# Performance work log

Measured on AMD Instinct MI355X. Metric: run time of the kernel, lower is better.

## Reference

```python
import jax, jax.numpy as jnp
import numpy as np

N = 50000       # nodes
E = 800000      # directed edges (src -> dst)
INDIM, HID, OUT = 256, 128, 64
NEG_SLOPE = 0.2  # PyG GATConv default negative_slope


def gat_layer(x, src, dst, W, a_src, a_dst, b, n_nodes):
    """Single-head PyG-style GATConv with self-loops already in (src, dst)."""
    h = x @ W.T                                   # [N, F_out]
    alpha_src = h @ a_src                         # [N]
    alpha_dst = h @ a_dst                         # [N]
    # per-edge attention logits, LeakyReLU
    e = jax.nn.leaky_relu(alpha_src[src] + alpha_dst[dst], NEG_SLOPE)  # [E']
    # segment softmax grouped by destination node (numerically stable)
    m = jnp.full((n_nodes,), -jnp.inf, e.dtype).at[dst].max(e)
    ee = jnp.exp(e - m[dst])
    denom = jax.ops.segment_sum(ee, dst, num_segments=n_nodes)
    alpha = ee / denom[dst]                       # [E']
    # weighted scatter-add of source messages
    out = jax.ops.segment_sum(h[src] * alpha[:, None], dst, num_segments=n_nodes)
    return out + b


def setup_inputs() -> dict:
    key = jax.random.key(0)
    ks = jax.random.split(key, 10)
    s = 0.1
    return {
        "x": jax.random.normal(ks[0], (N, INDIM), jnp.float32),
        "edge_index": jax.random.randint(ks[1], (2, E), 0, N, dtype=jnp.int32),
        "W1": jax.random.normal(ks[2], (HID, INDIM), jnp.float32) * s,
        "a_src1": jax.random.normal(ks[3], (HID,), jnp.float32) * s,
        "a_dst1": jax.random.normal(ks[4], (HID,), jnp.float32) * s,
        "b1": jnp.zeros((HID,), jnp.float32),
        "W2": jax.random.normal(ks[5], (OUT, HID), jnp.float32) * s,
        "a_src2": jax.random.normal(ks[6], (OUT,), jnp.float32) * s,
        "a_dst2": jax.random.normal(ks[7], (OUT,), jnp.float32) * s,
        "b2": jnp.zeros((OUT,), jnp.float32),
    }


def reference(x, edge_index, W1, a_src1, a_dst1, b1, W2, a_src2, a_dst2, b2):
    n_nodes = x.shape[0]
    # PyG GATConv default add_self_loops=True
    loops = jnp.arange(n_nodes, dtype=edge_index.dtype)
    src = jnp.concatenate([edge_index[0], loops])
    dst = jnp.concatenate([edge_index[1], loops])
    h = gat_layer(x, src, dst, W1, a_src1, a_dst1, b1, n_nodes)
    h = jax.nn.relu(h)
    h = gat_layer(h, src, dst, W2, a_src2, a_dst2, b2, n_nodes)
    return h
```

## Files before the change

### kernel.cpp

```cpp
#include <hip/hip_runtime.h>
#include <hip/hip_bf16.h>
#include <math.h>

#define NN 50000
#define EE 800000
#define INDIM 256
#define HID 128
#define OUTF 64
#define NEG_SLOPE 0.2f
#define CAP 64

#define NB ((NN + 255) >> 8)
#define BCAP 6144
#define CHUNK 2048
#define EPT 8
#define BPAD 16

typedef __attribute__((ext_vector_type(8))) short bf16x8;
typedef __attribute__((ext_vector_type(4))) float f32x4;

__device__ inline float bflo(unsigned p) { return __uint_as_float(p << 16); }
__device__ inline float bfhi(unsigned p) { return __uint_as_float(p & 0xffff0000u); }
__device__ inline unsigned f2bf(float f) {
    unsigned u = __float_as_uint(f);
    return (u + 0x7fffu + ((u >> 16) & 1u)) >> 16;
}
__device__ inline unsigned cvt_pk_bf16(float lo, float hi) {
    unsigned r;
    asm("v_cvt_pk_bf16_f32 %0, %1, %2" : "=v"(r) : "v"(lo), "v"(hi));
    return r;
}
__device__ inline float leaky(float l) { return (l > 0.f) ? l : NEG_SLOPE * l; }

template <typename AT, int BM, int BN, int WR, int WC, bool FAL>
__device__ inline void gemm_body(const AT* __restrict__ A,
                                 const float* __restrict__ B,
                                 unsigned short* __restrict__ Cb,
                                 const float* __restrict__ a_s,
                                 const float* __restrict__ a_d,
                                 float* __restrict__ asrc,
                                 float* __restrict__ adst,
                                 int N, int K, int bid)
{
    constexpr int LD = 40;
    constexpr int MF = (BM / WR) / 16;
    constexpr int NF = (BN / WC) / 16;
    constexpr int NA  = (sizeof(AT) == 4) ? (BM * 8 / 256) : (BM * 4 / 256);
    constexpr int NBL = BN * 8 / 256;
    __shared__ unsigned short As[BM * LD];
    __shared__ unsigned short Bs[BN * LD];
    __shared__ float al_s[FAL ? 2 * BM : 2];

    const int tid = threadIdx.x;
    const int wave = tid >> 6, lane = tid & 63;
    const int wr = wave / WC, wc = wave % WC;
    const int wrow0 = wr * (BM / WR);
    const int wcol0 = wc * (BN / WC);
    const int row0 = bid * BM;
    const int lrow = lane & 15, lkg = lane >> 4;

    if constexpr (FAL) {
        for (int i = tid; i < 2 * BM; i += 256) al_s[i] = 0.f;
    }

    int arow[NA], aoff[NA]; bool aval[NA];
    #pragma unroll
    for (int u = 0; u < NA; ++u) {
        int i = u * 256 + tid;
        if constexpr (sizeof(AT) == 4) { arow[u] = i >> 3; aoff[u] = (i & 7) * 4; }
        else                           { arow[u] = i >> 2; aoff[u] = (i & 3) * 8; }
        aval[u] = (row0 + arow[u]) < N;
    }
    int brow[NBL], boff[NBL];
    #pragma unroll
    for (int u = 0; u < NBL; ++u) {
        int i = u * 256 + tid;
        brow[u] = i >> 3; boff[u] = (i & 7) * 4;
    }

    uint4 ra[NA], rb[NBL];
    auto loadA = [&](int k0) {
        #pragma unroll
        for (int u = 0; u < NA; ++u) {
            ra[u] = make_uint4(0u, 0u, 0u, 0u);
            if (aval[u])
                ra[u] = *(const uint4*)((const AT*)A + (size_t)(row0 + arow[u]) * K + k0 + aoff[u]);
        }
    };
    auto loadB = [&](int k0) {
        #pragma unroll
        for (int u = 0; u < NBL; ++u)
            rb[u] = *(const uint4*)(B + (size_t)brow[u] * K + k0 + boff[u]);
    };
    auto storeLDS = [&]() {
        if constexpr (sizeof(AT) == 4) {
            #pragma unroll
            for (int u = 0; u < NA; ++u) {
                unsigned p0 = cvt_pk_bf16(__uint_as_float(ra[u].x), __uint_as_float(ra[u].y));
                unsigned p1 = cvt_pk_bf16(__uint_as_float(ra[u].z), __uint_as_float(ra[u].w));
                *(uint2*)&As[arow[u] * LD + aoff[u]] = make_uint2(p0, p1);
            }
        } else {
            #pragma unroll
            for (int u = 0; u < NA; ++u)
                *(uint4*)&As[arow[u] * LD + aoff[u]] = ra[u];
        }
        #pragma unroll
        for (int u = 0; u < NBL; ++u) {
            unsigned p0 = cvt_pk_bf16(__uint_as_float(rb[u].x), __uint_as_float(rb[u].y));
            unsigned p1 = cvt_pk_bf16(__uint_as_float(rb[u].z), __uint_as_float(rb[u].w));
            *(uint2*)&Bs[brow[u] * LD + boff[u]] = make_uint2(p0, p1);
        }
    };

    f32x4 acc[MF][NF];
    #pragma unroll
    for (int mi = 0; mi < MF; ++mi)
        #pragma unroll
        for (int ni = 0; ni < NF; ++ni) acc[mi][ni] = 0.f;

    const int NK = K / 32;
    loadA(0); loadB(0);
    for (int ks = 0; ks < NK; ++ks) {
        storeLDS();
        __syncthreads();
        if (ks + 1 < NK) { loadA((ks + 1) * 32); loadB((ks + 1) * 32); }

        bf16x8 af[MF], bfr[NF];
        #pragma unroll
        for (int mi = 0; mi < MF; ++mi)
            af[mi] = *(const bf16x8*)&As[(wrow0 + mi * 16 + lrow) * LD + lkg * 8];
        #pragma unroll
        for (int ni = 0; ni < NF; ++ni)
            bfr[ni] = *(const bf16x8*)&Bs[(wcol0 + ni * 16 + lrow) * LD + lkg * 8];
        #pragma unroll
        for (int mi = 0; mi < MF; ++mi)
            #pragma unroll
            for (int ni = 0; ni < NF; ++ni)
                acc[mi][ni] = __builtin_amdgcn_mfma_f32_16x16x32_bf16(
                    af[mi], bfr[ni], acc[mi][ni], 0, 0, 0);
        __syncthreads();
    }

    if constexpr (FAL) {
        float asv[NF], adv[NF];
        #pragma unroll
        for (int ni = 0; ni < NF; ++ni) {
            int c = wcol0 + ni * 16 + lrow;
            asv[ni] = a_s[c]; adv[ni] = a_d[c];
        }
        #pragma unroll
        for (int mi = 0; mi < MF; ++mi)
            #pragma unroll
            for (int r = 0; r < 4; ++r) {
                float ps = 0.f, pd = 0.f;
                #pragma unroll
                for (int ni = 0; ni < NF; ++ni) {
                    ps = fmaf(acc[mi][ni][r], asv[ni], ps);
                    pd = fmaf(acc[mi][ni][r], adv[ni], pd);
                }
                #pragma unroll
                for (int d = 1; d < 16; d <<= 1) {
                    ps += __shfl_xor(ps, d);
                    pd += __shfl_xor(pd, d);
                }
                int lr_ = wrow0 + mi * 16 + lkg * 4 + r;
                if (lrow == 0) {
                    atomicAdd(&al_s[lr_], ps);
                    atomicAdd(&al_s[BM + lr_], pd);
                }
            }
    }

    #pragma unroll
    for (int mi = 0; mi < MF; ++mi)
        #pragma unroll
        for (int ni = 0; ni < NF; ++ni)
            #pragma unroll
            for (int r = 0; r < 4; ++r) {
                int gr = row0 + wrow0 + mi * 16 + lkg * 4 + r;
                int gc = wcol0 + ni * 16 + lrow;
                if (gr < N)
                    Cb[(size_t)gr * BN + gc] = (unsigned short)f2bf(acc[mi][ni][r]);
            }

    if constexpr (FAL) {
        __syncthreads();
        if (tid < BM) {
            int gr = row0 + tid;
            if (gr < N) { asrc[gr] = al_s[tid]; adst[gr] = al_s[BM + tid]; }
        }
    }
}

__device__ inline void bin_body(int bb,
                                const int* __restrict__ src_in,
                                const int* __restrict__ dst_in,
                                unsigned* __restrict__ gbucket,
                                int* __restrict__ bcnt,
                                int E, int tot)
{
    __shared__ int h_hist[256];
    __shared__ int h_scan[256];
    __shared__ int h_ofs[256];
    __shared__ int h_gbase[256];
    __shared__ unsigned grp[CHUNK];

    const int tid = threadIdx.x;
    const int e0 = bb * CHUNK;
    const int cntc = min(CHUNK, tot - e0);

    h_hist[tid] = 0;
    __syncthreads();

    unsigned pk[EPT];
    bool val[EPT];
    #pragma unroll
    for (int u = 0; u < EPT; ++u) {
        int e = e0 + u * 256 + tid;
        val[u] = (e < tot);
        if (val[u]) {
            int d, s;
            if (e < E) { d = dst_in[e]; s = src_in[e]; }
            else       { d = e - E;    s = d; }
            pk[u] = ((unsigned)d << 16) | (unsigned)s;
            atomicAdd(&h_hist[d >> 8], 1);
        }
    }
    __syncthreads();

    int v = h_hist[tid];
    int incl = v;
    h_scan[tid] = incl;
    __syncthreads();
    for (int off = 1; off < 256; off <<= 1) {
        int t = (tid >= off) ? h_scan[tid - off] : 0;
        __syncthreads();
        incl += t;
        h_scan[tid] = incl;
        __syncthreads();
    }
    int excl = incl - v;
    h_scan[tid] = excl;
    h_ofs[tid] = excl;
    h_gbase[tid] = (tid < NB && v > 0) ? atomicAdd(&bcnt[tid * BPAD], v) : 0;
    __syncthreads();

    #pragma unroll
    for (int u = 0; u < EPT; ++u)
        if (val[u]) {
            int b = pk[u] >> 24;
            int pos = atomicAdd(&h_ofs[b], 1);
            grp[pos] = pk[u];
        }
    __syncthreads();

    for (int i = tid; i < cntc; i += 256) {
        unsigned p = grp[i];
        int b = p >> 24;
        int gp = h_gbase[b] + (i - h_scan[b]);
        if (gp < BCAP) gbucket[(size_t)b * BCAP + gp] = p;
    }
}

__global__ __launch_bounds__(256) void fused_gemm1_bin(
    const float* __restrict__ x, const float* __restrict__ W1,
    unsigned short* __restrict__ h1b,
    const float* __restrict__ a_s, const float* __restrict__ a_d,
    float* __restrict__ asrc, float* __restrict__ adst,
    const int* __restrict__ src_in, const int* __restrict__ dst_in,
    unsigned* __restrict__ gbucket, int* __restrict__ bcnt,
    int N, int K, int GB, int E)
{
    if ((int)blockIdx.x < GB) {
        gemm_body<float, 64, 128, 2, 2, true>(x, W1, h1b, a_s, a_d,
                                              asrc, adst, N, K, blockIdx.x);
    } else {
        bin_body(blockIdx.x - GB, src_in, dst_in, gbucket, bcnt, E, E + N);
    }
}

__global__ __launch_bounds__(256) void csr_build(
    const unsigned* __restrict__ gbucket, const int* __restrict__ bcnt,
    const float* __restrict__ asrc1, const float* __restrict__ adst1,
    int* __restrict__ cnt, unsigned short* __restrict__ csr,
    float* __restrict__ wcsr, int N)
{
    __shared__ int c2[256];
    __shared__ float den[256];
    __shared__ float ads[256];
    __shared__ unsigned short cl[256 * CAP];
    __shared__ float el[256 * CAP];

    const int b = blockIdx.x;
    const int tid = threadIdx.x;
    const int dg = (b << 8) + tid;
    c2[tid] = 0;
    den[tid] = 0.f;
    ads[tid] = (dg < N) ? adst1[dg] : 0.f;
    __syncthreads();

    int len = bcnt[b * BPAD];
    if (len > BCAP) len = BCAP;
    for (int i = tid; i < len; i += 256) {
        unsigned p = gbucket[(size_t)b * BCAP + i];
        int dl = (p >> 16) & 255;
        int s  = p & 0xffff;
        float e = __expf(leaky(asrc1[s] + ads[dl]));
        int r = atomicAdd(&c2[dl], 1);
        if (r < CAP) {
            cl[(dl << 6) + r] = (unsigned short)s;
            el[(dl << 6) + r] = e;
        }
        atomicAdd(&den[dl], e);
    }
    __syncthreads();

    if (dg < N) cnt[dg] = c2[tid];

    int rows = N - (b << 8);
    rows = (rows > 256) ? 256 : rows;

    for (int i = tid; i < rows * CAP; i += 256)
        el[i] = __fdividef(el[i], den[i >> 6]);
    __syncthreads();

    const uint4* sp = (const uint4*)cl;
    uint4* dp = (uint4*)(csr + (((size_t)b << 8) << 6));
    for (int i = tid; i < rows * 8; i += 256) dp[i] = sp[i];
    const uint4* wp = (const uint4*)el;
    uint4* dq = (uint4*)(wcsr + (((size_t)b << 8) << 6));
    for (int i = tid; i < rows * 16; i += 256) dq[i] = wp[i];
}

__global__ __launch_bounds__(256) void agg1_gemm2_kernel(
    const unsigned short* __restrict__ h1b, const unsigned short* __restrict__ csr,
    const int* __restrict__ cnt_arr, const float* __restrict__ wcsr,
    const float* __restrict__ b1,
    const float* __restrict__ W2, const float* __restrict__ a_s2,
    const float* __restrict__ a_d2, unsigned short* __restrict__ h2b,
    float* __restrict__ asrc2, float* __restrict__ adst2, int N)
{
    constexpr int F = HID, G = 16, EPI = 4, STEP = 16;
    constexpr int LDH = 136;
    __shared__ unsigned short hm[32 * LDH];
    __shared__ unsigned short Bs[64 * 40];
    __shared__ float al2[64];

    const int tid = threadIdx.x;
    const int wv = tid >> 6, lane = tid & 63;
    const int base = (int)blockIdx.x * 32;
    const int grp = lane / G, fl = lane % G;

    if (tid < 64) al2[tid] = 0.f;

    float bs[8];
    *(float4*)&bs[0] = *(const float4*)(b1 + fl * 8);
    *(float4*)&bs[4] = *(const float4*)(b1 + fl * 8 + 4);

    for (int i = 0; i < 8; ++i) {
        const int row = i * 4 + wv;
        const int node = base + row;
        float acc[8];
        #pragma unroll
        for (int p = 0; p < 8; ++p) acc[p] = 0.f;

        if (node < N) {
            const size_t beg = (size_t)node << 6;
            int cntv = cnt_arr[node];
            cntv = (cntv > CAP) ? CAP : cntv;

            int s = 0;
            float w = 0.f;
            if (lane < cntv) { s = (int)csr[beg + lane]; w = wcsr[beg + lane]; }

            for (int jj0 = 0; jj0 < cntv; jj0 += STEP) {
                uint4 q[4];
                float wj[4];
                #pragma unroll
                for (int u = 0; u < 4; ++u) {
                    int sel = jj0 + u * EPI + grp;
                    int sj = __shfl(s, sel);
                    wj[u] = __shfl(w, sel);
                    q[u] = make_uint4(0u, 0u, 0u, 0u);
                    if (sel < cntv)
                        q[u] = *(const uint4*)(h1b + (size_t)sj * F + fl * 8);
                }
                #pragma unroll
                for (int u = 0; u < 4; ++u) {
                    acc[0] += wj[u] * bflo(q[u].x); acc[1] += wj[u] * bfhi(q[u].x);
                    acc[2] += wj[u] * bflo(q[u].y); acc[3] += wj[u] * bfhi(q[u].y);
                    acc[4] += wj[u] * bflo(q[u].z); acc[5] += wj[u] * bfhi(q[u].z);
                    acc[6] += wj[u] * bflo(q[u].w); acc[7] += wj[u] * bfhi(q[u].w);
                }
            }
            #pragma unroll
            for (int d = G; d < 64; d <<= 1)
                #pragma unroll
                for (int p = 0; p < 8; ++p) acc[p] += __shfl_xor(acc[p], d);

            #pragma unroll
            for (int p = 0; p < 8; ++p) acc[p] = fmaxf(acc[p] + bs[p], 0.f);
        }
        if (lane < G) {
            uint4 pk;
            pk.x = cvt_pk_bf16(acc[0], acc[1]);
            pk.y = cvt_pk_bf16(acc[2], acc[3]);
            pk.z = cvt_pk_bf16(acc[4], acc[5]);
            pk.w = cvt_pk_bf16(acc[6], acc[7]);
            *(uint4*)&hm[row * LDH + lane * 8] = pk;
        }
    }
    __syncthreads();

    const int wr = wv >> 1, wc = wv & 1;
    const int lrow = lane & 15, lkg = lane >> 4;
    f32x4 acc2[2];
    #pragma unroll
    for (int ni = 0; ni < 2; ++ni) acc2[ni] = 0.f;

    for (int k0 = 0; k0 < HID; k0 += 32) {
        #pragma unroll
        for (int it = tid; it < 64 * 8; it += 256) {
            int rw = it >> 3, kq = it & 7;
            float4 v = *(const float4*)(W2 + (size_t)rw * HID + k0 + kq * 4);
            unsigned p0 = cvt_pk_bf16(v.x, v.y);
            unsigned p1 = cvt_pk_bf16(v.z, v.w);
            *(uint2*)&Bs[rw * 40 + kq * 4] = make_uint2(p0, p1);
        }
        __syncthreads();
        bf16x8 af = *(const bf16x8*)&hm[(wr * 16 + lrow) * LDH + k0 + lkg * 8];
        #pragma unroll
        for (int ni = 0; ni < 2; ++ni) {
            bf16x8 bfr = *(const bf16x8*)&Bs[(wc * 32 + ni * 16 + lrow) * 40 + lkg * 8];
            acc2[ni] = __builtin_amdgcn_mfma_f32_16x16x32_bf16(af, bfr, acc2[ni], 0, 0, 0);
        }
        __syncthreads();
    }

    float asv[2], adv[2];
    #pragma unroll
    for (int ni = 0; ni < 2; ++ni) {
        int c = wc * 32 + ni * 16 + lrow;
        asv[ni] = a_s2[c]; adv[ni] = a_d2[c];
    }
    #pragma unroll
    for (int r = 0; r < 4; ++r) {
        float ps = 0.f, pd = 0.f;
        #pragma unroll
        for (int ni = 0; ni < 2; ++ni) {
            ps = fmaf(acc2[ni][r], asv[ni], ps);
            pd = fmaf(acc2[ni][r], adv[ni], pd);
        }
        #pragma unroll
        for (int d = 1; d < 16; d <<= 1) {
            ps += __shfl_xor(ps, d);
            pd += __shfl_xor(pd, d);
        }
        int lr_ = wr * 16 + lkg * 4 + r;
        if (lrow == 0) {
            atomicAdd(&al2[lr_], ps);
            atomicAdd(&al2[32 + lr_], pd);
        }
    }
    __syncthreads();
    if (tid < 32) {
        int gr = base + tid;
        if (gr < N) { asrc2[gr] = al2[tid]; adst2[gr] = al2[32 + tid]; }
    }

    #pragma unroll
    for (int ni = 0; ni < 2; ++ni)
        #pragma unroll
        for (int r = 0; r < 4; ++r) {
            int gr = base + wr * 16 + lkg * 4 + r;
            int gc = wc * 32 + ni * 16 + lrow;
            if (gr < N)
                h2b[(size_t)gr * OUTF + gc] = (unsigned short)f2bf(acc2[ni][r]);
        }
}

template <int F, bool RELU, bool OUTBF>
__global__ __launch_bounds__(256) void aggregate_kernel(
    const unsigned short* __restrict__ hb, const unsigned short* __restrict__ csr,
    const int* __restrict__ cnt_arr, const float* __restrict__ asrc,
    const float* __restrict__ adst, const float* __restrict__ bias,
    void* __restrict__ outv, int n)
{
    constexpr int G = F / 8;
    constexpr int EPI = 64 / G;
    constexpr int STEP = EPI * 4;
    int wave = (int)((blockIdx.x * (size_t)blockDim.x + threadIdx.x) >> 6);
    int lane = threadIdx.x & 63;
    if (wave >= n) return;
    const size_t beg = (size_t)wave << 6;
    int cntv = cnt_arr[wave];
    cntv = (cntv > CAP) ? CAP : cntv;
    const float ad = adst[wave];
    const int grp = lane / G, fl = lane % G;

    float acc[8];
    #pragma unroll
    for (int p = 0; p < 8; ++p) acc[p] = 0.f;

    int s = 0;
    float e = 0.f;
    if (lane < cntv) { s = (int)csr[beg + lane]; e = __expf(leaky(asrc[s] + ad)); }
    float denom = e;
    #pragma unroll
    for (int d = 32; d > 0; d >>= 1) denom += __shfl_xor(denom, d);
    float w = e * __fdividef(1.f, denom);

    for (int jj0 = 0; jj0 < cntv; jj0 += STEP) {
        uint4 q[4];
        float wj[4];
        #pragma unroll
        for (int u = 0; u < 4; ++u) {
            int sel = jj0 + u * EPI + grp;
            int sj = __shfl(s, sel);
            wj[u] = __shfl(w, sel);
            q[u] = make_uint4(0u, 0u, 0u, 0u);
            if (sel < cntv)
                q[u] = *(const uint4*)(hb + (size_t)sj * F + fl * 8);
        }
        #pragma unroll
        for (int u = 0; u < 4; ++u) {
            acc[0] += wj[u] * bflo(q[u].x); acc[1] += wj[u] * bfhi(q[u].x);
            acc[2] += wj[u] * bflo(q[u].y); acc[3] += wj[u] * bfhi(q[u].y);
            acc[4] += wj[u] * bflo(q[u].z); acc[5] += wj[u] * bfhi(q[u].z);
            acc[6] += wj[u] * bflo(q[u].w); acc[7] += wj[u] * bfhi(q[u].w);
        }
    }

    #pragma unroll
    for (int d = G; d < 64; d <<= 1)
        #pragma unroll
        for (int p = 0; p < 8; ++p) acc[p] += __shfl_xor(acc[p], d);

    if (lane < G) {
        float v[8];
        #pragma unroll
        for (int p = 0; p < 8; ++p) {
            v[p] = acc[p] + bias[fl * 8 + p];
            if (RELU) v[p] = fmaxf(v[p], 0.f);
        }
        if constexpr (OUTBF) {
            unsigned short* o = (unsigned short*)outv + (size_t)wave * F + fl * 8;
            uint4 pk;
            pk.x = cvt_pk_bf16(v[0], v[1]);
            pk.y = cvt_pk_bf16(v[2], v[3]);
            pk.z = cvt_pk_bf16(v[4], v[5]);
            pk.w = cvt_pk_bf16(v[6], v[7]);
            *(uint4*)o = pk;
        } else {
            float* o = (float*)outv + (size_t)wave * F + fl * 8;
            *(float4*)o       = make_float4(v[0], v[1], v[2], v[3]);
            *(float4*)(o + 4) = make_float4(v[4], v[5], v[6], v[7]);
        }
    }
}

extern "C" void kernel_launch(void* const* d_in, const int* in_sizes, int n_in,
                              void* d_out, int out_size, void* d_ws, size_t ws_size,
                              hipStream_t stream)
{
    const float* x      = (const float*)d_in[0];
    const int*   ei     = (const int*)d_in[1];
    const float* W1     = (const float*)d_in[2];
    const float* a_src1 = (const float*)d_in[3];
    const float* a_dst1 = (const float*)d_in[4];
    const float* b1     = (const float*)d_in[5];
    const float* W2     = (const float*)d_in[6];
    const float* a_src2 = (const float*)d_in[7];
    const float* a_dst2 = (const float*)d_in[8];
    const float* b2     = (const float*)d_in[9];
    float* out = (float*)d_out;

    const int N = NN, E = EE;
    const int* src_in = ei;
    const int* dst_in = ei + E;

    char* p = (char*)d_ws;
    unsigned short* h1b   = (unsigned short*)p; p += (size_t)N * HID * 2;
    unsigned short* h2b   = (unsigned short*)p; p += (size_t)N * OUTF * 2;
    float* asrc  = (float*)p; p += (size_t)N * 4;
    float* adst  = (float*)p; p += (size_t)N * 4;
    float* asrc2 = (float*)p; p += (size_t)N * 4;
    float* adst2 = (float*)p; p += (size_t)N * 4;
    int* cnt    = (int*)p;   p += (size_t)N * 4;
    unsigned short* csr = (unsigned short*)p; p += (size_t)N * CAP * 2;
    float* wcsr = (float*)p; p += (size_t)N * CAP * 4;
    int* bcnt = (int*)p; p += (size_t)NB * BPAD * 4;
    unsigned* gbucket = (unsigned*)h2b;

    hipMemsetAsync(bcnt, 0, (size_t)NB * BPAD * 4, stream);

    const int GB   = (N + 63) / 64;
    const int BINB = (E + N + CHUNK - 1) / CHUNK;
    const int GBA  = (N + 31) / 32;
    const int nwb  = (N * 64 + 255) / 256;

    fused_gemm1_bin<<<GB + BINB, 256, 0, stream>>>(
        x, W1, h1b, a_src1, a_dst1, asrc, adst, src_in, dst_in,
        gbucket, bcnt, N, INDIM, GB, E);
    csr_build<<<NB, 256, 0, stream>>>(gbucket, bcnt, asrc, adst,
                                      cnt, csr, wcsr, N);

    agg1_gemm2_kernel<<<GBA, 256, 0, stream>>>(
        h1b, csr, cnt, wcsr, b1, W2, a_src2, a_dst2,
        h2b, asrc2, adst2, N);

    aggregate_kernel<OUTF, false, false><<<nwb, 256, 0, stream>>>(
        h2b, csr, cnt, asrc2, adst2, b2, out, N);

    (void)in_sizes; (void)n_in; (void)out_size; (void)ws_size;
}
```

Baseline: 209.3 us.

## Move layer-1 softmax into aggregation and issue all neighbor loads upfront

The softmax weight computation for layer 1 moves out of csr_build, which no longer needs large float shared arrays or the wcsr buffer write and read. Weights are now computed inside the aggregation kernel. Both aggregation kernels issue all neighbor-row gathers up front in a fully unrolled register array (up to CAP entries), overlapping the gather latency with the exp and denominator reduction. This raises register pressure because of the 16-entry uint4 array, and it always executes the full unrolled load and FMA sequence with predication rather than stopping at the neighbor count.

```diff
diff --git a/kernel.cpp b/kernel.cpp
--- a/kernel.cpp
+++ b/kernel.cpp
@@ -282,22 +282,14 @@
 
 __global__ __launch_bounds__(256) void csr_build(
     const unsigned* __restrict__ gbucket, const int* __restrict__ bcnt,
-    const float* __restrict__ asrc1, const float* __restrict__ adst1,
-    int* __restrict__ cnt, unsigned short* __restrict__ csr,
-    float* __restrict__ wcsr, int N)
+    int* __restrict__ cnt, unsigned short* __restrict__ csr, int N)
 {
     __shared__ int c2[256];
-    __shared__ float den[256];
-    __shared__ float ads[256];
     __shared__ unsigned short cl[256 * CAP];
-    __shared__ float el[256 * CAP];
 
     const int b = blockIdx.x;
     const int tid = threadIdx.x;
-    const int dg = (b << 8) + tid;
     c2[tid] = 0;
-    den[tid] = 0.f;
-    ads[tid] = (dg < N) ? adst1[dg] : 0.f;
     __syncthreads();
 
     int len = bcnt[b * BPAD];
@@ -306,42 +298,30 @@
         unsigned p = gbucket[(size_t)b * BCAP + i];
         int dl = (p >> 16) & 255;
         int s  = p & 0xffff;
-        float e = __expf(leaky(asrc1[s] + ads[dl]));
         int r = atomicAdd(&c2[dl], 1);
-        if (r < CAP) {
-            cl[(dl << 6) + r] = (unsigned short)s;
-            el[(dl << 6) + r] = e;
-        }
-        atomicAdd(&den[dl], e);
-    }
-    __syncthreads();
-
-    if (dg < N) cnt[dg] = c2[tid];
+        if (r < CAP) cl[(dl << 6) + r] = (unsigned short)s;
+    }
+    __syncthreads();
+
+    int d = (b << 8) + tid;
+    if (d < N) cnt[d] = c2[tid];
 
     int rows = N - (b << 8);
     rows = (rows > 256) ? 256 : rows;
-
-    for (int i = tid; i < rows * CAP; i += 256)
-        el[i] = __fdividef(el[i], den[i >> 6]);
-    __syncthreads();
-
     const uint4* sp = (const uint4*)cl;
     uint4* dp = (uint4*)(csr + (((size_t)b << 8) << 6));
     for (int i = tid; i < rows * 8; i += 256) dp[i] = sp[i];
-    const uint4* wp = (const uint4*)el;
-    uint4* dq = (uint4*)(wcsr + (((size_t)b << 8) << 6));
-    for (int i = tid; i < rows * 16; i += 256) dq[i] = wp[i];
 }
 
 __global__ __launch_bounds__(256) void agg1_gemm2_kernel(
     const unsigned short* __restrict__ h1b, const unsigned short* __restrict__ csr,
-    const int* __restrict__ cnt_arr, const float* __restrict__ wcsr,
-    const float* __restrict__ b1,
+    const int* __restrict__ cnt_arr, const float* __restrict__ asrc1,
+    const float* __restrict__ adst1, const float* __restrict__ b1,
     const float* __restrict__ W2, const float* __restrict__ a_s2,
     const float* __restrict__ a_d2, unsigned short* __restrict__ h2b,
     float* __restrict__ asrc2, float* __restrict__ adst2, int N)
 {
-    constexpr int F = HID, G = 16, EPI = 4, STEP = 16;
+    constexpr int F = HID, G = 16;
     constexpr int LDH = 136;
     __shared__ unsigned short hm[32 * LDH];
     __shared__ unsigned short Bs[64 * 40];
@@ -361,47 +341,54 @@
     for (int i = 0; i < 8; ++i) {
         const int row = i * 4 + wv;
         const int node = base + row;
+        const size_t beg = (size_t)node << 6;
+
+        int cntv = 0;
+        float ad = 0.f;
+        if (node < N) {
+            cntv = cnt_arr[node];
+            cntv = (cntv > CAP) ? CAP : cntv;
+            ad = adst1[node];
+        }
+        int s = 0;
+        if (lane < cntv) s = (int)csr[beg + lane];
+
+        uint4 q[16];
+        #pragma unroll
+        for (int u = 0; u < 16; ++u) {
+            int sel = u * 4 + grp;
+            int sj = __shfl(s, sel);
+            q[u] = make_uint4(0u, 0u, 0u, 0u);
+            if (sel < cntv)
+                q[u] = *(const uint4*)(h1b + (size_t)sj * F + fl * 8);
+        }
+
+        float e = 0.f;
+        if (lane < cntv) e = __expf(leaky(asrc1[s] + ad));
+        float denom = e;
+        #pragma unroll
+        for (int d = 32; d > 0; d >>= 1) denom += __shfl_xor(denom, d);
+        float w = (lane < cntv) ? e * __fdividef(1.f, denom) : 0.f;
+
         float acc[8];
         #pragma unroll
         for (int p = 0; p < 8; ++p) acc[p] = 0.f;
-
-        if (node < N) {
-            const size_t beg = (size_t)node << 6;
-            int cntv = cnt_arr[node];
-            cntv = (cntv > CAP) ? CAP : cntv;
-
-            int s = 0;
-            float w = 0.f;
-            if (lane < cntv) { s = (int)csr[beg + lane]; w = wcsr[beg + lane]; }
-
-            for (int jj0 = 0; jj0 < cntv; jj0 += STEP) {
-                uint4 q[4];
-                float wj[4];
-                #pragma unroll
-                for (int u = 0; u < 4; ++u) {
-                    int sel = jj0 + u * EPI + grp;
-                    int sj = __shfl(s, sel);
-                    wj[u] = __shfl(w, sel);
-                    q[u] = make_uint4(0u, 0u, 0u, 0u);
-                    if (sel < cntv)
-                        q[u] = *(const uint4*)(h1b + (size_t)sj * F + fl * 8);
-                }
-                #pragma unroll
-                for (int u = 0; u < 4; ++u) {
-                    acc[0] += wj[u] * bflo(q[u].x); acc[1] += wj[u] * bfhi(q[u].x);
-                    acc[2] += wj[u] * bflo(q[u].y); acc[3] += wj[u] * bfhi(q[u].y);
-                    acc[4] += wj[u] * bflo(q[u].z); acc[5] += wj[u] * bfhi(q[u].z);
-                    acc[6] += wj[u] * bflo(q[u].w); acc[7] += wj[u] * bfhi(q[u].w);
-                }
-            }
+        #pragma unroll
+        for (int u = 0; u < 16; ++u) {
+            float wj = __shfl(w, u * 4 + grp);
+            acc[0] += wj * bflo(q[u].x); acc[1] += wj * bfhi(q[u].x);
+            acc[2] += wj * bflo(q[u].y); acc[3] += wj * bfhi(q[u].y);
+            acc[4] += wj * bflo(q[u].z); acc[5] += wj * bfhi(q[u].z);
+            acc[6] += wj * bflo(q[u].w); acc[7] += wj * bfhi(q[u].w);
+        }
+        #pragma unroll
+        for (int d = G; d < 64; d <<= 1)
             #pragma unroll
-            for (int d = G; d < 64; d <<= 1)
-                #pragma unroll
-                for (int p = 0; p < 8; ++p) acc[p] += __shfl_xor(acc[p], d);
-
-            #pragma unroll
-            for (int p = 0; p < 8; ++p) acc[p] = fmaxf(acc[p] + bs[p], 0.f);
-        }
+            for (int p = 0; p < 8; ++p) acc[p] += __shfl_xor(acc[p], d);
+
+        #pragma unroll
+        for (int p = 0; p < 8; ++p) acc[p] = fmaxf(acc[p] + bs[p], 0.f);
+
         if (lane < G) {
             uint4 pk;
             pk.x = cvt_pk_bf16(acc[0], acc[1]);
@@ -489,7 +476,7 @@
 {
     constexpr int G = F / 8;
     constexpr int EPI = 64 / G;
-    constexpr int STEP = EPI * 4;
+    constexpr int NLD = 64 / EPI;
     int wave = (int)((blockIdx.x * (size_t)blockDim.x + threadIdx.x) >> 6);
     int lane = threadIdx.x & 63;
     if (wave >= n) return;
@@ -499,37 +486,36 @@
     const float ad = adst[wave];
     const int grp = lane / G, fl = lane % G;
 
+    int s = 0;
+    if (lane < cntv) s = (int)csr[beg + lane];
+
+    uint4 q[NLD];
+    #pragma unroll
+    for (int u = 0; u < NLD; ++u) {
+        int sel = u * EPI + grp;
+        int sj = __shfl(s, sel);
+        q[u] = make_uint4(0u, 0u, 0u, 0u);
+        if (sel < cntv)
+            q[u] = *(const uint4*)(hb + (size_t)sj * F + fl * 8);
+    }
+
+    float e = 0.f;
+    if (lane < cntv) e = __expf(leaky(asrc[s] + ad));
+    float denom = e;
+    #pragma unroll
+    for (int d = 32; d > 0; d >>= 1) denom += __shfl_xor(denom, d);
+    float w = (lane < cntv) ? e * __fdividef(1.f, denom) : 0.f;
+
     float acc[8];
     #pragma unroll
     for (int p = 0; p < 8; ++p) acc[p] = 0.f;
-
-    int s = 0;
-    float e = 0.f;
-    if (lane < cntv) { s = (int)csr[beg + lane]; e = __expf(leaky(asrc[s] + ad)); }
-    float denom = e;
-    #pragma unroll
-    for (int d = 32; d > 0; d >>= 1) denom += __shfl_xor(denom, d);
-    float w = e * __fdividef(1.f, denom);
-
-    for (int jj0 = 0; jj0 < cntv; jj0 += STEP) {
-        uint4 q[4];
-        float wj[4];
-        #pragma unroll
-        for (int u = 0; u < 4; ++u) {
-            int sel = jj0 + u * EPI + grp;
-            int sj = __shfl(s, sel);
-            wj[u] = __shfl(w, sel);
-            q[u] = make_uint4(0u, 0u, 0u, 0u);
-            if (sel < cntv)
-                q[u] = *(const uint4*)(hb + (size_t)sj * F + fl * 8);
-        }
-        #pragma unroll
-        for (int u = 0; u < 4; ++u) {
-            acc[0] += wj[u] * bflo(q[u].x); acc[1] += wj[u] * bfhi(q[u].x);
-            acc[2] += wj[u] * bflo(q[u].y); acc[3] += wj[u] * bfhi(q[u].y);
-            acc[4] += wj[u] * bflo(q[u].z); acc[5] += wj[u] * bfhi(q[u].z);
-            acc[6] += wj[u] * bflo(q[u].w); acc[7] += wj[u] * bfhi(q[u].w);
-        }
+    #pragma unroll
+    for (int u = 0; u < NLD; ++u) {
+        float wj = __shfl(w, u * EPI + grp);
+        acc[0] += wj * bflo(q[u].x); acc[1] += wj * bfhi(q[u].x);
+        acc[2] += wj * bflo(q[u].y); acc[3] += wj * bfhi(q[u].y);
+        acc[4] += wj * bflo(q[u].z); acc[5] += wj * bfhi(q[u].z);
+        acc[6] += wj * bflo(q[u].w); acc[7] += wj * bfhi(q[u].w);
     }
 
     #pragma unroll
@@ -589,7 +575,6 @@
     float* adst2 = (float*)p; p += (size_t)N * 4;
     int* cnt    = (int*)p;   p += (size_t)N * 4;
     unsigned short* csr = (unsigned short*)p; p += (size_t)N * CAP * 2;
-    float* wcsr = (float*)p; p += (size_t)N * CAP * 4;
     int* bcnt = (int*)p; p += (size_t)NB * BPAD * 4;
     unsigned* gbucket = (unsigned*)h2b;
 
@@ -603,11 +588,10 @@
     fused_gemm1_bin<<<GB + BINB, 256, 0, stream>>>(
         x, W1, h1b, a_src1, a_dst1, asrc, adst, src_in, dst_in,
         gbucket, bcnt, N, INDIM, GB, E);
-    csr_build<<<NB, 256, 0, stream>>>(gbucket, bcnt, asrc, adst,
-                                      cnt, csr, wcsr, N);
+    csr_build<<<NB, 256, 0, stream>>>(gbucket, bcnt, cnt, csr, N);
 
     agg1_gemm2_kernel<<<GBA, 256, 0, stream>>>(
-        h1b, csr, cnt, wcsr, b1, W2, a_src2, a_dst2,
+        h1b, csr, cnt, asrc, adst, b1, W2, a_src2, a_dst2,
         h2b, asrc2, adst2, N);
 
     aggregate_kernel<OUTF, false, false><<<nwb, 256, 0, stream>>>(
```

New measurement: 235.0 us. 1.12x slower.
